# Kernel optimization log

Measured on AMD Instinct MI355X. Metric: run time of the kernel, lower is better.

## Reference

```python
import jax, jax.numpy as jnp
import numpy as np

EPS = 1e-4  # Moller-Trumbore epsilon from the original

def _dot(a, b):
    return jnp.sum(a * b, axis=-1)

def setup_inputs() -> dict:
    key = jax.random.key(0)
    k1, k2, k3 = jax.random.split(key, 3)
    N, V, F = 2048, 2500, 4096
    p = jax.random.normal(k1, (N, 3), dtype=jnp.float32)
    v = jax.random.normal(k2, (V, 3), dtype=jnp.float32)
    f = jax.random.randint(k3, (F, 3), 0, V, dtype=jnp.int64)
    return {"p": p, "v": v, "f": f}

def reference(p, v, f):
    N = p.shape[0]
    faces = v[f]                      # (F,3,3)
    a, b, c = faces[:, 0], faces[:, 1], faces[:, 2]   # (F,3) each
    pe = p[None]                      # (1,N,3), broadcasts against (F,1,3)

    # --- point-to-triangle distance = min over the 3 edge segments (matches original output math) ---
    e1 = a - b                        # faces[:,0]-faces[:,1]
    e2 = c - b
    e3 = c - a

    def seg(e, ref_pt, q0, q1):
        # s = ((ref_pt - p) . e) / |e|^2, clamped; closest = s*q0 + (1-s)*q1  (original formula kept verbatim)
        m2 = _dot(e, e)[:, None]                       # (F,1)
        s = jnp.clip(_dot(ref_pt[:, None] - pe, e[:, None]) / m2, 0.0, 1.0)[..., None]  # (F,N,1)
        cl = s * q0[:, None] + (1.0 - s) * q1[:, None]  # (F,N,3)
        d = jnp.linalg.norm(cl - pe, axis=-1)           # (F,N)
        return d, cl

    d12, c12 = seg(e1, a, b, a)   # s12 from (p0-p).e1; closest = s*p1+(1-s)*p0
    d23, c23 = seg(e2, c, b, c)   # s23 from (p2-p).e2; closest = s*p1+(1-s)*p2
    d31, c31 = seg(e3, c, a, c)   # s31 from (p2-p).e3; closest = s*p0+(1-s)*p2

    d_all = jnp.stack([d12, d23, d31], axis=0)          # (3,F,N)
    c_all = jnp.stack([c12, c23, c31], axis=0)          # (3,F,N,3)
    which = jnp.argmin(d_all, axis=0)                   # (F,N)
    dist = jnp.min(d_all, axis=0)                       # (F,N)
    closest = jnp.take_along_axis(c_all, which[None, ..., None], axis=0)[0]  # (F,N,3)

    # nearest face per query point
    fidx = jnp.argmin(jnp.abs(dist), axis=0)            # (N,)
    dmin = jnp.take_along_axis(dist, fidx[None], axis=0)  # (1,N)
    closest_p = closest[fidx, jnp.arange(N)]            # (N,3)

    # --- Moller-Trumbore ray-triangle parity test toward mesh centroid ---
    dirv = v.mean(axis=0)[None] - p                     # (N,3)
    me1 = b - a                                         # faces[:,1]-faces[:,0]
    me2 = c - a
    pvec = jnp.cross(dirv[None], me2[:, None])          # (F,N,3)
    det = _dot(me1[:, None], pvec)                      # (F,N)
    tvec = pe - a[:, None]                              # (F,N,3)
    u = _dot(tvec, pvec) / det
    qvec = jnp.cross(tvec, me1[:, None])                # (F,N,3)
    dd = _dot(dirv[None], qvec) / det
    t = _dot(me2[:, None], qvec) / det
    hit = (jnp.abs(det) > EPS) & (u >= 0) & (u <= 1) & (dd >= 0) & (u + dd <= 1) & (t > EPS)
    counts = jnp.sum(hit, axis=0)                       # (N,)
    inside = (0.5 - (counts % 2 == 1).astype(dmin.dtype)) * 2.0  # +1 outside, -1 inside

    dmin = dmin * inside[None]                          # (1,N)
    return (dmin, closest_p)
```

## Files before the change

kernel.cpp:

```cpp
#include <hip/hip_runtime.h>
#include <math.h>

#define TRI_EPS 1e-4f

__global__ __launch_bounds__(256) void prep_kernel(
    const float* __restrict__ v, const int* __restrict__ f,
    float4* __restrict__ fdat6, float4* __restrict__ fdat5,
    float* __restrict__ vm, int V, int F) {
    const int t = threadIdx.x;
    const int j = blockIdx.x * 256 + t;
    if (j < F) {
        const int i0 = f[3 * j + 0];
        const int i1 = f[3 * j + 1];
        const int i2 = f[3 * j + 2];
        const float ax = v[3 * i0 + 0], ay = v[3 * i0 + 1], az = v[3 * i0 + 2];
        const float bx = v[3 * i1 + 0], by = v[3 * i1 + 1], bz = v[3 * i1 + 2];
        const float cx = v[3 * i2 + 0], cy = v[3 * i2 + 1], cz = v[3 * i2 + 2];
        const float e1x = ax - bx, e1y = ay - by, e1z = az - bz;
        const float e2x = cx - bx, e2y = cy - by, e2z = cz - bz;
        const float e3x = cx - ax, e3y = cy - ay, e3z = cz - az;
        const float m1 = e1x * e1x + e1y * e1y + e1z * e1z;
        const float m2 = e2x * e2x + e2y * e2y + e2z * e2z;
        const float m3 = e3x * e3x + e3y * e3y + e3z * e3z;
        const float inv1 = 1.f / m1, inv2 = 1.f / m2, inv3 = 1.f / m3;
        fdat6[6 * j + 0] = make_float4(ax, ay, az, inv1);
        fdat6[6 * j + 1] = make_float4(bx, by, bz, inv2);
        fdat6[6 * j + 2] = make_float4(cx, cy, cz, inv3);
        fdat6[6 * j + 3] = make_float4(e1x, e1y, e1z, 0.f);
        fdat6[6 * j + 4] = make_float4(e2x, e2y, e2z, 0.f);
        fdat6[6 * j + 5] = make_float4(e3x, e3y, e3z, 0.f);
        fdat5[5 * j + 0] = make_float4(ax, ay, az, inv1);
        fdat5[5 * j + 1] = make_float4(cx, cy, cz, inv2);
        fdat5[5 * j + 2] = make_float4(e1x, e1y, e1z, inv3);
        fdat5[5 * j + 3] = make_float4(e2x, e2y, e2z, 0.f);
        fdat5[5 * j + 4] = make_float4(e3x, e3y, e3z, 0.f);
    }
    if (blockIdx.x == 0) {
        __shared__ float sx[256], sy[256], sz[256];
        float x = 0.f, y = 0.f, z = 0.f;
        for (int i = t; i < V; i += 256) {
            x += v[3 * i + 0];
            y += v[3 * i + 1];
            z += v[3 * i + 2];
        }
        sx[t] = x; sy[t] = y; sz[t] = z;
        __syncthreads();
        for (int off = 128; off > 0; off >>= 1) {
            if (t < off) {
                sx[t] += sx[t + off];
                sy[t] += sy[t + off];
                sz[t] += sz[t + off];
            }
            __syncthreads();
        }
        if (t == 0) {
            vm[0] = sx[0] / (float)V;
            vm[1] = sy[0] / (float)V;
            vm[2] = sz[0] / (float)V;
        }
    }
}

struct FP {
    float d1, d2, d3;
    float x1, y1, z1, x2, y2, z2, x3, y3, z3;
    float apx, apy, apz;
};

__device__ __forceinline__ FP face_point(
    const float4 ra, const float4 rb, const float4 rc,
    const float e1x, const float e1y, const float e1z,
    const float e2x, const float e2y, const float e2z,
    const float e3x, const float e3y, const float e3z,
    const float px, const float py, const float pz) {
    FP r;
    const float ax = ra.x, ay = ra.y, az = ra.z;
    const float bx = rb.x, by = rb.y, bz = rb.z;
    const float cx = rc.x, cy = rc.y, cz = rc.z;
    r.apx = ax - px; r.apy = ay - py; r.apz = az - pz;
    const float cpx = cx - px, cpy = cy - py, cpz = cz - pz;

    float s1 = (r.apx * e1x + r.apy * e1y + r.apz * e1z) * ra.w;
    s1 = fminf(fmaxf(s1, 0.f), 1.f);
    const float o1 = 1.f - s1;
    r.x1 = s1 * bx + o1 * ax;
    r.y1 = s1 * by + o1 * ay;
    r.z1 = s1 * bz + o1 * az;
    float ux = r.x1 - px, uy = r.y1 - py, uz = r.z1 - pz;
    r.d1 = ux * ux + uy * uy + uz * uz;

    float s2 = (cpx * e2x + cpy * e2y + cpz * e2z) * rb.w;
    s2 = fminf(fmaxf(s2, 0.f), 1.f);
    const float o2 = 1.f - s2;
    r.x2 = s2 * bx + o2 * cx;
    r.y2 = s2 * by + o2 * cy;
    r.z2 = s2 * bz + o2 * cz;
    ux = r.x2 - px; uy = r.y2 - py; uz = r.z2 - pz;
    r.d2 = ux * ux + uy * uy + uz * uz;

    float s3 = (cpx * e3x + cpy * e3y + cpz * e3z) * rc.w;
    s3 = fminf(fmaxf(s3, 0.f), 1.f);
    const float o3 = 1.f - s3;
    r.x3 = s3 * ax + o3 * cx;
    r.y3 = s3 * ay + o3 * cy;
    r.z3 = s3 * az + o3 * cz;
    ux = r.x3 - px; uy = r.y3 - py; uz = r.z3 - pz;
    r.d3 = ux * ux + uy * uy + uz * uz;
    return r;
}

__device__ __forceinline__ void pair_lean(
    const float4 r0, const float4 r1, const float4 r2,
    const float4 r3, const float4 r4,
    const float px, const float py, const float pz,
    const float dx, const float dy, const float dz, const int j,
    float& bd2, int& bid, int& hits) {
    const float apx = r0.x - px, apy = r0.y - py, apz = r0.z - pz;
    const float cpx = r1.x - px, cpy = r1.y - py, cpz = r1.z - pz;
    const float e1x = r2.x, e1y = r2.y, e1z = r2.z;
    const float e2x = r3.x, e2y = r3.y, e2z = r3.z;
    const float e3x = r4.x, e3y = r4.y, e3z = r4.z;

    float s1 = (apx * e1x + apy * e1y + apz * e1z) * r0.w;
    s1 = fminf(fmaxf(s1, 0.f), 1.f);
    const float u1x = apx - s1 * e1x;
    const float u1y = apy - s1 * e1y;
    const float u1z = apz - s1 * e1z;
    const float d1 = u1x * u1x + u1y * u1y + u1z * u1z;

    float s2 = (cpx * e2x + cpy * e2y + cpz * e2z) * r1.w;
    s2 = fminf(fmaxf(s2, 0.f), 1.f);
    const float u2x = cpx - s2 * e2x;
    const float u2y = cpy - s2 * e2y;
    const float u2z = cpz - s2 * e2z;
    const float d2 = u2x * u2x + u2y * u2y + u2z * u2z;

    float s3 = (cpx * e3x + cpy * e3y + cpz * e3z) * r2.w;
    s3 = fminf(fmaxf(s3, 0.f), 1.f);
    const float u3x = cpx - s3 * e3x;
    const float u3y = cpy - s3 * e3y;
    const float u3z = cpz - s3 * e3z;
    const float d3 = u3x * u3x + u3y * u3y + u3z * u3z;

    float fd2 = d1; int eid = 0;
    if (d2 < fd2) { fd2 = d2; eid = 1; }
    if (d3 < fd2) { fd2 = d3; eid = 2; }
    if (fd2 < bd2) { bd2 = fd2; bid = (j << 2) | eid; }

    const float pvx = dy * e3z - dz * e3y;
    const float pvy = dz * e3x - dx * e3z;
    const float pvz = dx * e3y - dy * e3x;
    const float det = -(e1x * pvx + e1y * pvy + e1z * pvz);
    const float tu = -(apx * pvx + apy * pvy + apz * pvz);
    const float qvx = apy * e1z - apz * e1y;
    const float qvy = apz * e1x - apx * e1z;
    const float qvz = apx * e1y - apy * e1x;
    const float td = dx * qvx + dy * qvy + dz * qvz;
    const float tn = e3x * qvx + e3y * qvy + e3z * qvz;
    const float adet = fabsf(det);
    const float sd = (det > 0.f) ? 1.f : -1.f;
    const float su = tu * sd;
    const float sq = td * sd;
    const float st = tn * sd;
    if (adet > TRI_EPS && su >= 0.f && su <= adet && sq >= 0.f &&
        (su + sq) <= adet && st > TRI_EPS * adet)
        hits++;
}

template <int CS>
__global__ __launch_bounds__(256) void sdf_main2_t(
    const float* __restrict__ p, const float4* __restrict__ fd5,
    const float* __restrict__ vm,
    unsigned long long* __restrict__ keysP, unsigned* __restrict__ hitsP,
    int N, int C) {
    __shared__ float4 sfd[5 * CS];
    const int t = threadIdx.x;
    const int k = blockIdx.x % C;
    const int pg = blockIdx.x / C;
    const int j0 = k * CS;

    if (t < 5 * CS) sfd[t] = fd5[5 * j0 + t];

    const int iA = pg * 512 + t;
    const int iB = iA + 256;
    const bool vA = (iA < N);
    const bool vB = (iB < N);
    const int lA = vA ? iA : 0;
    const int lB = vB ? iB : 0;
    const float pAx = p[3 * lA + 0], pAy = p[3 * lA + 1], pAz = p[3 * lA + 2];
    const float pBx = p[3 * lB + 0], pBy = p[3 * lB + 1], pBz = p[3 * lB + 2];
    const float vmx = vm[0], vmy = vm[1], vmz = vm[2];
    const float dAx = vmx - pAx, dAy = vmy - pAy, dAz = vmz - pAz;
    const float dBx = vmx - pBx, dBy = vmy - pBy, dBz = vmz - pBz;

    float Ad2 = INFINITY; int Aid = 0x7fffffff; int Ah = 0;
    float Bd2 = INFINITY; int Bid = 0x7fffffff; int Bh = 0;

    __syncthreads();

    #pragma unroll 2
    for (int jj = 0; jj < CS; ++jj) {
        const float4 r0 = sfd[5 * jj + 0];
        const float4 r1 = sfd[5 * jj + 1];
        const float4 r2 = sfd[5 * jj + 2];
        const float4 r3 = sfd[5 * jj + 3];
        const float4 r4 = sfd[5 * jj + 4];
        const int j = j0 + jj;
        pair_lean(r0, r1, r2, r3, r4, pAx, pAy, pAz, dAx, dAy, dAz, j,
                  Ad2, Aid, Ah);
        pair_lean(r0, r1, r2, r3, r4, pBx, pBy, pBz, dBx, dBy, dBz, j,
                  Bd2, Bid, Bh);
    }

    if (vA) {
        keysP[(size_t)k * N + iA] =
            ((unsigned long long)__float_as_uint(Ad2) << 32) | (unsigned int)Aid;
        hitsP[(size_t)k * N + iA] = (unsigned)Ah;
    }
    if (vB) {
        keysP[(size_t)k * N + iB] =
            ((unsigned long long)__float_as_uint(Bd2) << 32) | (unsigned int)Bid;
        hitsP[(size_t)k * N + iB] = (unsigned)Bh;
    }
}

__global__ __launch_bounds__(256) void sdf_main_g(
    const float* __restrict__ p, const float4* __restrict__ fd5,
    const float* __restrict__ vm,
    unsigned long long* __restrict__ keysP, unsigned* __restrict__ hitsP,
    int N, int F, int C, int CS) {
    const int k = blockIdx.x % C;
    const int pg = blockIdx.x / C;
    const int i = pg * 256 + threadIdx.x;
    if (i >= N) return;
    const float px = p[3 * i + 0];
    const float py = p[3 * i + 1];
    const float pz = p[3 * i + 2];
    const float dx = vm[0] - px;
    const float dy = vm[1] - py;
    const float dz = vm[2] - pz;
    float bd2 = INFINITY; int bid = 0x7fffffff; int hits = 0;
    const int j0 = k * CS;
    const int j1 = min(F, j0 + CS);
    for (int j = j0; j < j1; ++j) {
        pair_lean(fd5[5 * j + 0], fd5[5 * j + 1], fd5[5 * j + 2],
                  fd5[5 * j + 3], fd5[5 * j + 4],
                  px, py, pz, dx, dy, dz, j, bd2, bid, hits);
    }
    keysP[(size_t)k * N + i] =
        ((unsigned long long)__float_as_uint(bd2) << 32) | (unsigned int)bid;
    hitsP[(size_t)k * N + i] = (unsigned)hits;
}

__global__ __launch_bounds__(256) void sdf_reduce_epi(
    const float* __restrict__ p, const float4* __restrict__ fd6,
    const unsigned long long* __restrict__ keysP,
    const unsigned* __restrict__ hitsP,
    float* __restrict__ out, int N, int C) {
    const int t = threadIdx.x;
    const int q = t & 63;
    const int w = t >> 6;
    const int i = blockIdx.x * 64 + q;

    unsigned long long bk = 0xFFFFFFFFFFFFFFFFull;
    unsigned hs = 0;
    if (i < N) {
        const int kpw = C >> 2;
        int k = w * kpw;
        #pragma unroll 4
        for (int kk = 0; kk < kpw; ++kk, ++k) {
            const unsigned long long kv = keysP[(size_t)k * N + i];
            if (kv < bk) bk = kv;
            hs += hitsP[(size_t)k * N + i];
        }
    }
    __shared__ unsigned long long sk[4][64];
    __shared__ unsigned sh[4][64];
    sk[w][q] = bk;
    sh[w][q] = hs;
    __syncthreads();
    if (w == 0 && i < N) {
        #pragma unroll
        for (int ww = 1; ww < 4; ++ww) {
            const unsigned long long kv = sk[ww][q];
            if (kv < bk) bk = kv;
            hs += sh[ww][q];
        }
        const float bd2 = __uint_as_float((unsigned int)(bk >> 32));
        const int bid = (int)(unsigned int)(bk & 0xFFFFFFFFull);
        const int jw = bid >> 2;
        const int eid = bid & 3;
        const float px = p[3 * i + 0];
        const float py = p[3 * i + 1];
        const float pz = p[3 * i + 2];
        const float4 wa  = fd6[6 * jw + 0];
        const float4 wb  = fd6[6 * jw + 1];
        const float4 wc  = fd6[6 * jw + 2];
        const float4 we1 = fd6[6 * jw + 3];
        const float4 we2 = fd6[6 * jw + 4];
        const float4 we3 = fd6[6 * jw + 5];
        const FP r = face_point(wa, wb, wc, we1.x, we1.y, we1.z,
                                we2.x, we2.y, we2.z, we3.x, we3.y, we3.z,
                                px, py, pz);
        float clx = r.x1, cly = r.y1, clz = r.z1;
        if (eid == 1) { clx = r.x2; cly = r.y2; clz = r.z2; }
        if (eid == 2) { clx = r.x3; cly = r.y3; clz = r.z3; }
        const float d = sqrtf(bd2);
        out[i] = (hs & 1u) ? -d : d;
        out[N + 3 * i + 0] = clx;
        out[N + 3 * i + 1] = cly;
        out[N + 3 * i + 2] = clz;
    }
}

extern "C" void kernel_launch(void* const* d_in, const int* in_sizes, int n_in,
                              void* d_out, int out_size, void* d_ws,
                              size_t ws_size, hipStream_t stream) {
    const float* p = (const float*)d_in[0];
    const float* v = (const float*)d_in[1];
    const int* f = (const int*)d_in[2];
    float* out = (float*)d_out;

    const int N = in_sizes[0] / 3;
    const int V = in_sizes[1] / 3;
    const int F = in_sizes[2] / 3;

    const int C = 512;
    const int CS = 8;

    char* base = (char*)d_ws;
    float* vm = (float*)base;
    unsigned long long* keysP = (unsigned long long*)(base + 16);
    unsigned* hitsP = (unsigned*)(base + 16 + 8ull * C * N);
    size_t off = 16 + 12ull * C * N;
    off = (off + 15) & ~15ull;
    float4* fdat6 = (float4*)(base + off);
    float4* fdat5 = (float4*)(base + off + 6ull * F * sizeof(float4));

    prep_kernel<<<(F + 255) / 256, 256, 0, stream>>>(v, f, fdat6, fdat5, vm,
                                                     V, F);

    if (F == C * CS) {
        const int npg = (N + 511) / 512;
        sdf_main2_t<CS><<<npg * C, 256, 0, stream>>>(p, fdat5, vm, keysP,
                                                     hitsP, N, C);
    } else {
        const int CSg = (F + C - 1) / C;
        const int npg = (N + 255) / 256;
        sdf_main_g<<<npg * C, 256, 0, stream>>>(p, fdat5, vm, keysP, hitsP,
                                                N, F, C, CSg);
    }
    sdf_reduce_epi<<<(N + 63) / 64, 256, 0, stream>>>(p, fdat6, keysP, hitsP,
                                                      out, N, C);
}
```

Baseline: 53.23 us.

## Process four points per thread, halve face chunks, widen partial reduction

The main kernel now handles four query points per thread (1024 per block) over 16-face chunks with 256 chunks, replacing two points per thread over 8-face chunks with 512 chunks. This gives more register-level reuse of each face loaded from shared memory and halves the partial-result buffer that the reduce kernel must read. The reduce kernel now uses 16 points per block with 16 chunk-strided lanes and a shared-memory tree reduction, which spreads the partial reads over more blocks. In exchange the main kernel uses more registers per thread and launches fewer blocks, so occupancy may drop.

```diff
diff --git a/kernel.cpp b/kernel.cpp
--- a/kernel.cpp
+++ b/kernel.cpp
@@ -2,6 +2,7 @@
 #include <math.h>
 
 #define TRI_EPS 1e-4f
+typedef unsigned long long u64;
 
 __global__ __launch_bounds__(256) void prep_kernel(
     const float* __restrict__ v, const int* __restrict__ f,
@@ -168,10 +169,10 @@
 }
 
 template <int CS>
-__global__ __launch_bounds__(256) void sdf_main2_t(
+__global__ __launch_bounds__(256) void sdf_main4(
     const float* __restrict__ p, const float4* __restrict__ fd5,
     const float* __restrict__ vm,
-    unsigned long long* __restrict__ keysP, unsigned* __restrict__ hitsP,
+    u64* __restrict__ keysP, unsigned* __restrict__ hitsP,
     int N, int C) {
     __shared__ float4 sfd[5 * CS];
     const int t = threadIdx.x;
@@ -181,24 +182,28 @@
 
     if (t < 5 * CS) sfd[t] = fd5[5 * j0 + t];
 
-    const int iA = pg * 512 + t;
-    const int iB = iA + 256;
-    const bool vA = (iA < N);
-    const bool vB = (iB < N);
-    const int lA = vA ? iA : 0;
-    const int lB = vB ? iB : 0;
-    const float pAx = p[3 * lA + 0], pAy = p[3 * lA + 1], pAz = p[3 * lA + 2];
-    const float pBx = p[3 * lB + 0], pBy = p[3 * lB + 1], pBz = p[3 * lB + 2];
     const float vmx = vm[0], vmy = vm[1], vmz = vm[2];
-    const float dAx = vmx - pAx, dAy = vmy - pAy, dAz = vmz - pAz;
-    const float dBx = vmx - pBx, dBy = vmy - pBy, dBz = vmz - pBz;
-
-    float Ad2 = INFINITY; int Aid = 0x7fffffff; int Ah = 0;
-    float Bd2 = INFINITY; int Bid = 0x7fffffff; int Bh = 0;
-
+    float px[4], py[4], pz[4], dx[4], dy[4], dz[4], bd2[4];
+    int bid[4], hh[4], idx[4];
+    bool vld[4];
+    #pragma unroll
+    for (int q = 0; q < 4; ++q) {
+        const int i = pg * 1024 + q * 256 + t;
+        idx[q] = i;
+        vld[q] = (i < N);
+        const int li = vld[q] ? i : 0;
+        px[q] = p[3 * li + 0];
+        py[q] = p[3 * li + 1];
+        pz[q] = p[3 * li + 2];
+        dx[q] = vmx - px[q];
+        dy[q] = vmy - py[q];
+        dz[q] = vmz - pz[q];
+        bd2[q] = INFINITY;
+        bid[q] = 0x7fffffff;
+        hh[q] = 0;
+    }
     __syncthreads();
 
-    #pragma unroll 2
     for (int jj = 0; jj < CS; ++jj) {
         const float4 r0 = sfd[5 * jj + 0];
         const float4 r1 = sfd[5 * jj + 1];
@@ -206,28 +211,27 @@
         const float4 r3 = sfd[5 * jj + 3];
         const float4 r4 = sfd[5 * jj + 4];
         const int j = j0 + jj;
-        pair_lean(r0, r1, r2, r3, r4, pAx, pAy, pAz, dAx, dAy, dAz, j,
-                  Ad2, Aid, Ah);
-        pair_lean(r0, r1, r2, r3, r4, pBx, pBy, pBz, dBx, dBy, dBz, j,
-                  Bd2, Bid, Bh);
-    }
-
-    if (vA) {
-        keysP[(size_t)k * N + iA] =
-            ((unsigned long long)__float_as_uint(Ad2) << 32) | (unsigned int)Aid;
-        hitsP[(size_t)k * N + iA] = (unsigned)Ah;
-    }
-    if (vB) {
-        keysP[(size_t)k * N + iB] =
-            ((unsigned long long)__float_as_uint(Bd2) << 32) | (unsigned int)Bid;
-        hitsP[(size_t)k * N + iB] = (unsigned)Bh;
+        #pragma unroll
+        for (int q = 0; q < 4; ++q) {
+            pair_lean(r0, r1, r2, r3, r4, px[q], py[q], pz[q],
+                      dx[q], dy[q], dz[q], j, bd2[q], bid[q], hh[q]);
+        }
+    }
+
+    #pragma unroll
+    for (int q = 0; q < 4; ++q) {
+        if (vld[q]) {
+            keysP[(size_t)k * N + idx[q]] =
+                ((u64)__float_as_uint(bd2[q]) << 32) | (unsigned)bid[q];
+            hitsP[(size_t)k * N + idx[q]] = (unsigned)hh[q];
+        }
     }
 }
 
 __global__ __launch_bounds__(256) void sdf_main_g(
     const float* __restrict__ p, const float4* __restrict__ fd5,
     const float* __restrict__ vm,
-    unsigned long long* __restrict__ keysP, unsigned* __restrict__ hitsP,
+    u64* __restrict__ keysP, unsigned* __restrict__ hitsP,
     int N, int F, int C, int CS) {
     const int k = blockIdx.x % C;
     const int pg = blockIdx.x / C;
@@ -248,46 +252,48 @@
                   px, py, pz, dx, dy, dz, j, bd2, bid, hits);
     }
     keysP[(size_t)k * N + i] =
-        ((unsigned long long)__float_as_uint(bd2) << 32) | (unsigned int)bid;
+        ((u64)__float_as_uint(bd2) << 32) | (unsigned)bid;
     hitsP[(size_t)k * N + i] = (unsigned)hits;
 }
 
-__global__ __launch_bounds__(256) void sdf_reduce_epi(
+__global__ __launch_bounds__(256) void sdf_reduce_epi16(
     const float* __restrict__ p, const float4* __restrict__ fd6,
-    const unsigned long long* __restrict__ keysP,
-    const unsigned* __restrict__ hitsP,
+    const u64* __restrict__ keysP, const unsigned* __restrict__ hitsP,
     float* __restrict__ out, int N, int C) {
     const int t = threadIdx.x;
-    const int q = t & 63;
-    const int w = t >> 6;
-    const int i = blockIdx.x * 64 + q;
-
-    unsigned long long bk = 0xFFFFFFFFFFFFFFFFull;
+    const int ii = t & 15;
+    const int ks = t >> 4;
+    const int i = blockIdx.x * 16 + ii;
+
+    u64 bk = 0xFFFFFFFFFFFFFFFFull;
     unsigned hs = 0;
     if (i < N) {
-        const int kpw = C >> 2;
-        int k = w * kpw;
-        #pragma unroll 4
-        for (int kk = 0; kk < kpw; ++kk, ++k) {
-            const unsigned long long kv = keysP[(size_t)k * N + i];
+        const int kspan = C >> 4;
+        for (int kk = 0; kk < kspan; ++kk) {
+            const int k = ks + kk * 16;
+            const u64 kv = keysP[(size_t)k * N + i];
             if (kv < bk) bk = kv;
             hs += hitsP[(size_t)k * N + i];
         }
     }
-    __shared__ unsigned long long sk[4][64];
-    __shared__ unsigned sh[4][64];
-    sk[w][q] = bk;
-    sh[w][q] = hs;
+    __shared__ u64 sk[16][17];
+    __shared__ unsigned sh[16][17];
+    sk[ks][ii] = bk;
+    sh[ks][ii] = hs;
     __syncthreads();
-    if (w == 0 && i < N) {
-        #pragma unroll
-        for (int ww = 1; ww < 4; ++ww) {
-            const unsigned long long kv = sk[ww][q];
-            if (kv < bk) bk = kv;
-            hs += sh[ww][q];
-        }
-        const float bd2 = __uint_as_float((unsigned int)(bk >> 32));
-        const int bid = (int)(unsigned int)(bk & 0xFFFFFFFFull);
+    for (int off = 8; off > 0; off >>= 1) {
+        if (ks < off) {
+            const u64 kv = sk[ks + off][ii];
+            if (kv < sk[ks][ii]) sk[ks][ii] = kv;
+            sh[ks][ii] += sh[ks + off][ii];
+        }
+        __syncthreads();
+    }
+    if (t < 16 && i < N) {
+        const u64 key = sk[0][t];
+        const unsigned hits = sh[0][t];
+        const float bd2 = __uint_as_float((unsigned)(key >> 32));
+        const int bid = (int)(unsigned)(key & 0xFFFFFFFFull);
         const int jw = bid >> 2;
         const int eid = bid & 3;
         const float px = p[3 * i + 0];
@@ -306,7 +312,7 @@
         if (eid == 1) { clx = r.x2; cly = r.y2; clz = r.z2; }
         if (eid == 2) { clx = r.x3; cly = r.y3; clz = r.z3; }
         const float d = sqrtf(bd2);
-        out[i] = (hs & 1u) ? -d : d;
+        out[i] = (hits & 1u) ? -d : d;
         out[N + 3 * i + 0] = clx;
         out[N + 3 * i + 1] = cly;
         out[N + 3 * i + 2] = clz;
@@ -325,12 +331,12 @@
     const int V = in_sizes[1] / 3;
     const int F = in_sizes[2] / 3;
 
-    const int C = 512;
-    const int CS = 8;
+    const int C = 256;
+    const int CS = 16;
 
     char* base = (char*)d_ws;
     float* vm = (float*)base;
-    unsigned long long* keysP = (unsigned long long*)(base + 16);
+    u64* keysP = (u64*)(base + 16);
     unsigned* hitsP = (unsigned*)(base + 16 + 8ull * C * N);
     size_t off = 16 + 12ull * C * N;
     off = (off + 15) & ~15ull;
@@ -341,15 +347,15 @@
                                                      V, F);
 
     if (F == C * CS) {
-        const int npg = (N + 511) / 512;
-        sdf_main2_t<CS><<<npg * C, 256, 0, stream>>>(p, fdat5, vm, keysP,
-                                                     hitsP, N, C);
+        const int pgs = (N + 1023) / 1024;
+        sdf_main4<16><<<pgs * C, 256, 0, stream>>>(p, fdat5, vm, keysP, hitsP,
+                                                   N, C);
     } else {
         const int CSg = (F + C - 1) / C;
         const int npg = (N + 255) / 256;
         sdf_main_g<<<npg * C, 256, 0, stream>>>(p, fdat5, vm, keysP, hitsP,
                                                 N, F, C, CSg);
     }
-    sdf_reduce_epi<<<(N + 63) / 64, 256, 0, stream>>>(p, fdat6, keysP, hitsP,
-                                                      out, N, C);
-}
+    sdf_reduce_epi16<<<(N + 15) / 16, 256, 0, stream>>>(p, fdat6, keysP, hitsP,
+                                                        out, N, C);
+}
```

New measurement: 43.84 us. 1.21x faster.
